# Optimization experiments

Measured on AMD Instinct MI355X. Metric: run time of the kernel, lower is better.

Reference implementation:

```python
import jax, jax.numpy as jnp
import numpy as np

BETA = 0.35

def setup_inputs() -> dict:
    key = jax.random.key(0)
    k1, k2, k3 = jax.random.split(key, 3)
    B, D, C, O = 16384, 512, 4096, 128
    x = jax.random.normal(k1, (B, D), dtype=jnp.float32)
    centers = jax.random.normal(k2, (C, D), dtype=jnp.float32)
    W = jax.random.normal(k3, (C, O), dtype=jnp.float32) * (1.0 / np.sqrt(C))
    b = jnp.zeros((O,), dtype=jnp.float32)
    return {"x": x, "centers": centers, "W": W, "b": b}

def reference(x, centers, W, b):
    # Squared Euclidean distances via the GEMM identity ||a-b||^2 = ||a||^2 + ||b||^2 - 2 a.b
    # (same math as expand_dims/subtract/square/reduce_sum, avoids [B,C,D] intermediate)
    x_sq = jnp.sum(x * x, axis=1, keepdims=True)          # [B,1]
    c_sq = jnp.sum(centers * centers, axis=1)             # [C]
    cross = x @ centers.T                                  # [B,C]
    sq_dist = x_sq + c_sq[None, :] - 2.0 * cross           # [B,C]
    rbf = jnp.exp(-BETA * sq_dist)                         # [B,C]
    return rbf @ W + b                                      # [B,O]
```

## Files before the change

kernel.cpp:

```cpp
#include <hip/hip_runtime.h>
#include <hip/hip_bf16.h>

typedef short bf16x8 __attribute__((ext_vector_type(8)));
typedef float f32x4 __attribute__((ext_vector_type(4)));
typedef float f32x16 __attribute__((ext_vector_type(16)));
typedef long l64x2 __attribute__((ext_vector_type(2)));
typedef unsigned short u16;
typedef unsigned char u8;

#define NB2 (-0.35f * 1.44269504088896340736f)
#define P2C (0.70f * 1.44269504088896340736f)
#define MF8(a,b,c)  __builtin_amdgcn_mfma_f32_32x32x16_fp8_fp8(a, b, c, 0, 0, 0)
#define MFB(a,b,c)  __builtin_amdgcn_mfma_f32_32x32x16_bf16(a, b, c, 0, 0, 0)

__device__ __forceinline__ u16 f2bf(float f) {
  union { float f; unsigned int u; } v; v.f = f;
  unsigned int x = v.u;
  return (u16)((x + 0x7FFFu + ((x >> 16) & 1u)) >> 16);
}

__device__ __forceinline__ unsigned cvtpk(float lo, float hi) {
  unsigned r;
  asm("v_cvt_pk_bf16_f32 %0, %1, %2" : "=v"(r) : "v"(lo), "v"(hi));
  return r;
}

__device__ __forceinline__ void pswap(unsigned &a, unsigned &b) {
  asm volatile("v_permlane32_swap_b32 %0, %1" : "+v"(a), "+v"(b));
}

__device__ __forceinline__ u8 f2e4m3(float f) {
  unsigned int u = __float_as_uint(f);
  u8 s = (u8)((u >> 24) & 0x80u);
  float a = fabsf(f);
  if (a >= 448.f) return s | 0x7E;
  if (a < 0.015625f) return s | (u8)(int)rintf(a * 512.f);
  unsigned int m = u & 0x7fffffffu;
  unsigned int r = m + 0x7FFFFu + ((m >> 20) & 1u);
  return s | (u8)((((r >> 23) - 120u) << 3) | ((r >> 20) & 7u));
}

__device__ __forceinline__ unsigned int pk4(float a, float b, float c, float d) {
#if __has_builtin(__builtin_amdgcn_cvt_pk_fp8_f32)
  int v = __builtin_amdgcn_cvt_pk_fp8_f32(a, b, 0, false);
  v = __builtin_amdgcn_cvt_pk_fp8_f32(c, d, v, true);
  return (unsigned int)v;
#else
  return (unsigned int)f2e4m3(a) | ((unsigned int)f2e4m3(b) << 8)
       | ((unsigned int)f2e4m3(c) << 16) | ((unsigned int)f2e4m3(d) << 24);
#endif
}

#define GLOAD_LDS(g, l) __builtin_amdgcn_global_load_lds( \
    (const __attribute__((address_space(1))) unsigned int*)(g), \
    (__attribute__((address_space(3))) unsigned int*)(l), 16, 0, 0)

__global__ __launch_bounds__(512)
void prep_x8(const float* __restrict__ src, u8* __restrict__ dst,
             float* __restrict__ sq) {
  const int row = blockIdx.x * 8 + (threadIdx.x >> 6);
  const int i6 = threadIdx.x & 63;
  const float4* p = (const float4*)(src + (size_t)row * 512) + i6 * 2;
  float4 a = p[0], b = p[1];
  float ss = a.x*a.x + a.y*a.y + a.z*a.z + a.w*a.w
           + b.x*b.x + b.y*b.y + b.z*b.z + b.w*b.w;
  uint2 o;
  o.x = pk4(a.x, a.y, a.z, a.w);
  o.y = pk4(b.x, b.y, b.z, b.w);
  const int pp = i6 >> 2, sub = (i6 >> 1) & 1, h = i6 & 1;
  const int l = (h << 5) | (row & 31);
  *(uint2*)(dst + (size_t)(row >> 5) * 16384 + pp * 1024 + l * 16 + sub * 8) = o;
  ss += __shfl_xor(ss, 1);  ss += __shfl_xor(ss, 2);
  ss += __shfl_xor(ss, 4);  ss += __shfl_xor(ss, 8);
  ss += __shfl_xor(ss, 16); ss += __shfl_xor(ss, 32);
  if (i6 == 0) sq[row] = ss;
}

__global__ __launch_bounds__(256)
void prep_cen(const float* __restrict__ cen, u8* __restrict__ cfr,
              float* __restrict__ csq) {
  const int t = threadIdx.x;
  const int c = blockIdx.x * 4 + (t >> 6);
  const int i6 = t & 63;
  const float* p = cen + (size_t)c * 512 + i6 * 8;
  float4 a = *(const float4*)p, b = *(const float4*)(p + 4);
  float ss = a.x*a.x + a.y*a.y + a.z*a.z + a.w*a.w
           + b.x*b.x + b.y*b.y + b.z*b.z + b.w*b.w;
  uint2 o;
  o.x = pk4(a.x, a.y, a.z, a.w);
  o.y = pk4(b.x, b.y, b.z, b.w);
  const int pp = i6 >> 2, sub = (i6 >> 1) & 1, h = i6 & 1;
  const int lc = c & 31;
  const int v = (((lc & 7) * 2 + h) ^ ((lc >> 2) & 1));
  *(uint2*)(cfr + (size_t)(c >> 5) * 16384 + pp * 1024 + (lc >> 3) * 256
            + v * 16 + sub * 8) = o;
  ss += __shfl_xor(ss, 1);  ss += __shfl_xor(ss, 2);
  ss += __shfl_xor(ss, 4);  ss += __shfl_xor(ss, 8);
  ss += __shfl_xor(ss, 16); ss += __shfl_xor(ss, 32);
  if (i6 == 0) csq[c] = ss;
}

__global__ __launch_bounds__(256)
void prep_w(const float* __restrict__ W, u8* __restrict__ wt) {
  __shared__ u16 t_[128 * 66];
  const int c0 = blockIdx.x * 64;
  const int t = threadIdx.x;
#pragma unroll
  for (int it = 0; it < 32; ++it) {
    int idx = it * 256 + t;
    int cl = idx >> 7;
    int o  = idx & 127;
    t_[o * 66 + cl] = f2bf(W[(size_t)(c0 + cl) * 128 + o]);
  }
  __syncthreads();
#pragma unroll
  for (int it = 0; it < 4; ++it) {
    int idx = it * 256 + t;
    int o  = idx >> 3;
    int uu = idx & 7;
    int ch = uu >> 2;
    int kt = (uu >> 1) & 1;
    int h  = uu & 1;
    u16* d = (u16*)(wt + ((size_t)(c0 >> 5) + ch) * 8192 + (o >> 5) * 2048
                    + kt * 1024 + (h * 32 + (o & 31)) * 16);
    const u16* s_ = &t_[o * 66 + ch * 32 + kt * 16 + h * 8];
#pragma unroll
    for (int j = 0; j < 8; ++j) d[j] = s_[j];
  }
}

__global__ __launch_bounds__(256)
void init_out(const float* __restrict__ bias, float* __restrict__ out) {
  const int i4 = blockIdx.x * 256 + threadIdx.x;
  float4 b = ((const float4*)bias)[i4 & 31];
  ((float4*)out)[i4] = b;
}

__global__ __launch_bounds__(256, 2)
void rbf_main(const u8* __restrict__ xfs, const u8* __restrict__ cfr,
              const u8* __restrict__ wtgb, const float* __restrict__ csq_g,
              const float* __restrict__ xsq_g, float* __restrict__ out)
{
  __shared__ __align__(16) u8 cs[3][16384];
  __shared__ __align__(16) float csq_l[1024];
  __shared__ __align__(16) float xsq_l[128];

  const int tid = threadIdx.x;
  const int lane = tid & 63;
  const int wv = tid >> 6;
  const int l31 = lane & 31;
  const int h = lane >> 5;
  const int bid = blockIdx.x;
  const int chq = bid & 3;
  const size_t r0 = (size_t)(bid >> 2) * 128;

#define S_CS(cc) do { \
    const u8* sG_ = cfr + ((size_t)(chq * 32 + (cc)) << 14) + tid * 16; \
    u8* sL_ = &cs[(cc) % 3][0] + tid * 16; \
    GLOAD_LDS(sG_,         sL_); \
    GLOAD_LDS(sG_ + 4096,  sL_ + 4096); \
    GLOAD_LDS(sG_ + 8192,  sL_ + 8192); \
    GLOAD_LDS(sG_ + 12288, sL_ + 12288); \
  } while (0)

  if (tid < 32) GLOAD_LDS(xsq_g + r0 + tid * 4, xsq_l + tid * 4);
  GLOAD_LDS(csq_g + chq * 1024 + tid * 4, csq_l + tid * 4);
  S_CS(0);
  S_CS(1);

  l64x2 xf[16];
  {
    const u8* xb = xfs + ((size_t)((bid >> 2) * 4 + wv)) * 16384 + lane * 16;
#pragma unroll
    for (int p = 0; p < 16; ++p)
      xf[p] = *(const l64x2*)(xb + p * 1024);
  }

  asm volatile("s_waitcnt vmcnt(0)" ::: "memory");
  __builtin_amdgcn_s_barrier();
  __builtin_amdgcn_sched_barrier(0);

  const float xn = NB2 * xsq_l[wv * 32 + l31];

  const int cbase = ((l31 >> 3) & 3) * 256
                  + ((((l31 & 7) * 2 + h) ^ ((l31 >> 2) & 1)) << 4);

  const f32x16 z16 = {0,0,0,0,0,0,0,0,0,0,0,0,0,0,0,0};
  f32x16 oa0 = z16, oa1 = z16, oa2 = z16, oa3 = z16;

#pragma unroll 1
  for (int cc = 0; cc < 32; ++cc) {
    const u8* wgb = wtgb + ((size_t)(chq * 32 + cc) << 13) + lane * 16;
    bf16x8 w00 = *(const bf16x8*)(wgb);
    bf16x8 w01 = *(const bf16x8*)(wgb + 1024);
    bf16x8 w10 = *(const bf16x8*)(wgb + 2048);
    bf16x8 w11 = *(const bf16x8*)(wgb + 3072);
    bf16x8 w20 = *(const bf16x8*)(wgb + 4096);
    bf16x8 w21 = *(const bf16x8*)(wgb + 5120);
    bf16x8 w30 = *(const bf16x8*)(wgb + 6144);
    bf16x8 w31 = *(const bf16x8*)(wgb + 7168);
    __builtin_amdgcn_sched_barrier(0);
    if (cc < 30) S_CS(cc + 2);
    __builtin_amdgcn_sched_barrier(0);

    const u8* csb = &cs[cc % 3][0];

    f32x16 s0 = z16, s1 = z16;
#pragma unroll
    for (int p = 0; p < 16; ++p) {
      l64x2 A = *(const l64x2*)(csb + p * 1024 + cbase);
      __builtin_amdgcn_s_setprio(1);
      if (p & 1) {
        s1 = MF8(A[0], xf[p][0], s1);
        s1 = MF8(A[1], xf[p][1], s1);
      } else {
        s0 = MF8(A[0], xf[p][0], s0);
        s0 = MF8(A[1], xf[p][1], s0);
      }
      __builtin_amdgcn_s_setprio(0);
    }

    f32x4 cq0 = *(const f32x4*)(csq_l + cc * 32 + 0  + 4 * h);
    f32x4 cq1 = *(const f32x4*)(csq_l + cc * 32 + 8  + 4 * h);
    f32x4 cq2 = *(const f32x4*)(csq_l + cc * 32 + 16 + 4 * h);
    f32x4 cq3 = *(const f32x4*)(csq_l + cc * 32 + 24 + 4 * h);
    float e[16];
#pragma unroll
    for (int r = 0; r < 16; ++r) {
      const float cq = (r < 4 ? cq0[r] : r < 8 ? cq1[r - 4] : r < 12 ? cq2[r - 8] : cq3[r - 12]);
      e[r] = __builtin_amdgcn_exp2f(fmaf(s0[r] + s1[r], P2C, fmaf(cq, NB2, xn)));
    }
    unsigned P0 = cvtpk(e[0],  e[1]),  P1 = cvtpk(e[2],  e[3]);
    unsigned P2 = cvtpk(e[4],  e[5]),  P3 = cvtpk(e[6],  e[7]);
    unsigned P4 = cvtpk(e[8],  e[9]),  P5 = cvtpk(e[10], e[11]);
    unsigned P6 = cvtpk(e[12], e[13]), P7 = cvtpk(e[14], e[15]);
    pswap(P0, P2); pswap(P1, P3);
    pswap(P4, P6); pswap(P5, P7);
    union { unsigned u[4]; bf16x8 v; } FA, GA;
    FA.u[0] = P0; FA.u[1] = P1; FA.u[2] = P2; FA.u[3] = P3;
    GA.u[0] = P4; GA.u[1] = P5; GA.u[2] = P6; GA.u[3] = P7;

    if (cc < 30) { asm volatile("s_waitcnt vmcnt(4)" ::: "memory"); }
    else         { asm volatile("s_waitcnt vmcnt(0)" ::: "memory"); }
    __builtin_amdgcn_sched_barrier(0);
    __builtin_amdgcn_s_setprio(1);
    oa0 = MFB(FA.v, w00, oa0);
    oa0 = MFB(GA.v, w01, oa0);
    oa1 = MFB(FA.v, w10, oa1);
    oa1 = MFB(GA.v, w11, oa1);
    oa2 = MFB(FA.v, w20, oa2);
    oa2 = MFB(GA.v, w21, oa2);
    oa3 = MFB(FA.v, w30, oa3);
    oa3 = MFB(GA.v, w31, oa3);
    __builtin_amdgcn_s_setprio(0);

    __builtin_amdgcn_s_barrier();
    __builtin_amdgcn_sched_barrier(0);
  }

#pragma unroll
  for (int r = 0; r < 16; ++r) {
    const int m = wv * 32 + (r & 3) + 8 * (r >> 2) + 4 * h;
    float* op = &out[(r0 + m) * 128 + l31];
    atomicAdd(op,      oa0[r]);
    atomicAdd(op + 32, oa1[r]);
    atomicAdd(op + 64, oa2[r]);
    atomicAdd(op + 96, oa3[r]);
  }
#undef S_CS
}

extern "C" void kernel_launch(void* const* d_in, const int* in_sizes, int n_in,
                              void* d_out, int out_size, void* d_ws, size_t ws_size,
                              hipStream_t stream) {
  (void)in_sizes; (void)n_in; (void)out_size; (void)ws_size;
  const float* x   = (const float*)d_in[0];
  const float* cen = (const float*)d_in[1];
  const float* W   = (const float*)d_in[2];
  const float* b   = (const float*)d_in[3];
  u8* xfs = (u8*)d_ws;
  u8* cfr = xfs + (size_t)16384 * 512;
  u8* wtgb = cfr + (size_t)4096 * 512;
  float* csq = (float*)(wtgb + (size_t)128 * 4096 * 2);
  float* xsq = csq + 4096;
  prep_x8<<<2048, 512, 0, stream>>>(x, xfs, xsq);
  prep_cen<<<1024, 256, 0, stream>>>(cen, cfr, csq);
  prep_w<<<64, 256, 0, stream>>>(W, wtgb);
  init_out<<<2048, 256, 0, stream>>>(b, (float*)d_out);
  rbf_main<<<512, 256, 0, stream>>>(xfs, cfr, wtgb, csq, xsq, (float*)d_out);
}
```

Measured before the change: 109.5 us.

## Software-pipeline distance GEMM of next chunk with exp and output GEMM

```diff
diff --git a/kernel.cpp b/kernel.cpp
--- a/kernel.cpp
+++ b/kernel.cpp
@@ -141,7 +141,7 @@
               const u8* __restrict__ wtgb, const float* __restrict__ csq_g,
               const float* __restrict__ xsq_g, float* __restrict__ out)
 {
-  __shared__ __align__(16) u8 cs[3][16384];
+  __shared__ __align__(16) u8 cs[4][16384];
   __shared__ __align__(16) float csq_l[1024];
   __shared__ __align__(16) float xsq_l[128];
 
@@ -156,7 +156,7 @@
 
 #define S_CS(cc) do { \
     const u8* sG_ = cfr + ((size_t)(chq * 32 + (cc)) << 14) + tid * 16; \
-    u8* sL_ = &cs[(cc) % 3][0] + tid * 16; \
+    u8* sL_ = &cs[(cc) & 3][0] + tid * 16; \
     GLOAD_LDS(sG_,         sL_); \
     GLOAD_LDS(sG_ + 4096,  sL_ + 4096); \
     GLOAD_LDS(sG_ + 8192,  sL_ + 8192); \
@@ -181,82 +181,101 @@
   __builtin_amdgcn_sched_barrier(0);
 
   const float xn = NB2 * xsq_l[wv * 32 + l31];
-
   const int cbase = ((l31 >> 3) & 3) * 256
                   + ((((l31 & 7) * 2 + h) ^ ((l31 >> 2) & 1)) << 4);
 
   const f32x16 z16 = {0,0,0,0,0,0,0,0,0,0,0,0,0,0,0,0};
   f32x16 oa0 = z16, oa1 = z16, oa2 = z16, oa3 = z16;
+  f32x16 sA0 = z16, sA1 = z16, sB0 = z16, sB1 = z16;
+
+#define G1Q(Na, Nb, Q, CSB, INIT) do { \
+    l64x2 A0 = *(const l64x2*)((CSB) + (4*(Q)+0)*1024 + cbase); \
+    l64x2 A1 = *(const l64x2*)((CSB) + (4*(Q)+1)*1024 + cbase); \
+    l64x2 A2 = *(const l64x2*)((CSB) + (4*(Q)+2)*1024 + cbase); \
+    l64x2 A3 = *(const l64x2*)((CSB) + (4*(Q)+3)*1024 + cbase); \
+    __builtin_amdgcn_s_setprio(1); \
+    if (INIT) { Na = MF8(A0[0], xf[4*(Q)+0][0], z16); \
+                Nb = MF8(A1[0], xf[4*(Q)+1][0], z16); } \
+    else      { Na = MF8(A0[0], xf[4*(Q)+0][0], Na); \
+                Nb = MF8(A1[0], xf[4*(Q)+1][0], Nb); } \
+    Na = MF8(A0[1], xf[4*(Q)+0][1], Na); \
+    Nb = MF8(A1[1], xf[4*(Q)+1][1], Nb); \
+    Na = MF8(A2[0], xf[4*(Q)+2][0], Na); \
+    Nb = MF8(A3[0], xf[4*(Q)+3][0], Nb); \
+    Na = MF8(A2[1], xf[4*(Q)+2][1], Na); \
+    Nb = MF8(A3[1], xf[4*(Q)+3][1], Nb); \
+    __builtin_amdgcn_s_setprio(0); \
+  } while (0)
+
+#define EXPQ(Ca, Cb, Q, CC, Pa, Pb) do { \
+    f32x4 cqv = *(const f32x4*)(csq_l + (CC) * 32 + (Q) * 8 + 4 * h); \
+    float e0_ = __builtin_amdgcn_exp2f(fmaf((Ca)[4*(Q)+0] + (Cb)[4*(Q)+0], P2C, fmaf(cqv[0], NB2, xn))); \
+    float e1_ = __builtin_amdgcn_exp2f(fmaf((Ca)[4*(Q)+1] + (Cb)[4*(Q)+1], P2C, fmaf(cqv[1], NB2, xn))); \
+    float e2_ = __builtin_amdgcn_exp2f(fmaf((Ca)[4*(Q)+2] + (Cb)[4*(Q)+2], P2C, fmaf(cqv[2], NB2, xn))); \
+    float e3_ = __builtin_amdgcn_exp2f(fmaf((Ca)[4*(Q)+3] + (Cb)[4*(Q)+3], P2C, fmaf(cqv[3], NB2, xn))); \
+    Pa = cvtpk(e0_, e1_); \
+    Pb = cvtpk(e2_, e3_); \
+  } while (0)
+
+#define BODY(CC, Ca, Cb, Na, Nb, VM) do { \
+    asm volatile("s_waitcnt vmcnt(0)" ::: "memory"); \
+    __builtin_amdgcn_s_barrier(); \
+    __builtin_amdgcn_sched_barrier(0); \
+    const u8* wgb = wtgb + ((size_t)(chq * 32 + (CC)) << 13) + lane * 16; \
+    bf16x8 w00 = *(const bf16x8*)(wgb); \
+    bf16x8 w01 = *(const bf16x8*)(wgb + 1024); \
+    bf16x8 w10 = *(const bf16x8*)(wgb + 2048); \
+    bf16x8 w11 = *(const bf16x8*)(wgb + 3072); \
+    bf16x8 w20 = *(const bf16x8*)(wgb + 4096); \
+    bf16x8 w21 = *(const bf16x8*)(wgb + 5120); \
+    bf16x8 w30 = *(const bf16x8*)(wgb + 6144); \
+    bf16x8 w31 = *(const bf16x8*)(wgb + 7168); \
+    if ((CC) + 2 < 32) S_CS((CC) + 2); \
+    __builtin_amdgcn_sched_barrier(0); \
+    const u8* csb = &cs[((CC) + 1) & 3][0]; \
+    unsigned P0, P1, P2, P3, P4, P5, P6, P7; \
+    if ((CC) < 31) G1Q(Na, Nb, 0, csb, 1); \
+    EXPQ(Ca, Cb, 0, CC, P0, P1); \
+    if ((CC) < 31) G1Q(Na, Nb, 1, csb, 0); \
+    EXPQ(Ca, Cb, 1, CC, P2, P3); \
+    if ((CC) < 31) G1Q(Na, Nb, 2, csb, 0); \
+    EXPQ(Ca, Cb, 2, CC, P4, P5); \
+    if ((CC) < 31) G1Q(Na, Nb, 3, csb, 0); \
+    EXPQ(Ca, Cb, 3, CC, P6, P7); \
+    pswap(P0, P2); pswap(P1, P3); \
+    pswap(P4, P6); pswap(P5, P7); \
+    union { unsigned u[4]; bf16x8 v; } FA, GA; \
+    FA.u[0] = P0; FA.u[1] = P1; FA.u[2] = P2; FA.u[3] = P3; \
+    GA.u[0] = P4; GA.u[1] = P5; GA.u[2] = P6; GA.u[3] = P7; \
+    asm volatile("s_waitcnt vmcnt(" #VM ")" ::: "memory"); \
+    __builtin_amdgcn_sched_barrier(0); \
+    __builtin_amdgcn_s_setprio(1); \
+    oa0 = MFB(FA.v, w00, oa0); \
+    oa1 = MFB(FA.v, w10, oa1); \
+    oa2 = MFB(FA.v, w20, oa2); \
+    oa3 = MFB(FA.v, w30, oa3); \
+    oa0 = MFB(GA.v, w01, oa0); \
+    oa1 = MFB(GA.v, w11, oa1); \
+    oa2 = MFB(GA.v, w21, oa2); \
+    oa3 = MFB(GA.v, w31, oa3); \
+    __builtin_amdgcn_s_setprio(0); \
+  } while (0)
+
+  {
+    const u8* csb0 = &cs[0][0];
+    G1Q(sA0, sA1, 0, csb0, 1);
+    G1Q(sA0, sA1, 1, csb0, 0);
+    G1Q(sA0, sA1, 2, csb0, 0);
+    G1Q(sA0, sA1, 3, csb0, 0);
+  }
 
 #pragma unroll 1
-  for (int cc = 0; cc < 32; ++cc) {
-    const u8* wgb = wtgb + ((size_t)(chq * 32 + cc) << 13) + lane * 16;
-    bf16x8 w00 = *(const bf16x8*)(wgb);
-    bf16x8 w01 = *(const bf16x8*)(wgb + 1024);
-    bf16x8 w10 = *(const bf16x8*)(wgb + 2048);
-    bf16x8 w11 = *(const bf16x8*)(wgb + 3072);
-    bf16x8 w20 = *(const bf16x8*)(wgb + 4096);
-    bf16x8 w21 = *(const bf16x8*)(wgb + 5120);
-    bf16x8 w30 = *(const bf16x8*)(wgb + 6144);
-    bf16x8 w31 = *(const bf16x8*)(wgb + 7168);
-    __builtin_amdgcn_sched_barrier(0);
-    if (cc < 30) S_CS(cc + 2);
-    __builtin_amdgcn_sched_barrier(0);
-
-    const u8* csb = &cs[cc % 3][0];
-
-    f32x16 s0 = z16, s1 = z16;
-#pragma unroll
-    for (int p = 0; p < 16; ++p) {
-      l64x2 A = *(const l64x2*)(csb + p * 1024 + cbase);
-      __builtin_amdgcn_s_setprio(1);
-      if (p & 1) {
-        s1 = MF8(A[0], xf[p][0], s1);
-        s1 = MF8(A[1], xf[p][1], s1);
-      } else {
-        s0 = MF8(A[0], xf[p][0], s0);
-        s0 = MF8(A[1], xf[p][1], s0);
-      }
-      __builtin_amdgcn_s_setprio(0);
-    }
-
-    f32x4 cq0 = *(const f32x4*)(csq_l + cc * 32 + 0  + 4 * h);
-    f32x4 cq1 = *(const f32x4*)(csq_l + cc * 32 + 8  + 4 * h);
-    f32x4 cq2 = *(const f32x4*)(csq_l + cc * 32 + 16 + 4 * h);
-    f32x4 cq3 = *(const f32x4*)(csq_l + cc * 32 + 24 + 4 * h);
-    float e[16];
-#pragma unroll
-    for (int r = 0; r < 16; ++r) {
-      const float cq = (r < 4 ? cq0[r] : r < 8 ? cq1[r - 4] : r < 12 ? cq2[r - 8] : cq3[r - 12]);
-      e[r] = __builtin_amdgcn_exp2f(fmaf(s0[r] + s1[r], P2C, fmaf(cq, NB2, xn)));
-    }
-    unsigned P0 = cvtpk(e[0],  e[1]),  P1 = cvtpk(e[2],  e[3]);
-    unsigned P2 = cvtpk(e[4],  e[5]),  P3 = cvtpk(e[6],  e[7]);
-    unsigned P4 = cvtpk(e[8],  e[9]),  P5 = cvtpk(e[10], e[11]);
-    unsigned P6 = cvtpk(e[12], e[13]), P7 = cvtpk(e[14], e[15]);
-    pswap(P0, P2); pswap(P1, P3);
-    pswap(P4, P6); pswap(P5, P7);
-    union { unsigned u[4]; bf16x8 v; } FA, GA;
-    FA.u[0] = P0; FA.u[1] = P1; FA.u[2] = P2; FA.u[3] = P3;
-    GA.u[0] = P4; GA.u[1] = P5; GA.u[2] = P6; GA.u[3] = P7;
-
-    if (cc < 30) { asm volatile("s_waitcnt vmcnt(4)" ::: "memory"); }
-    else         { asm volatile("s_waitcnt vmcnt(0)" ::: "memory"); }
-    __builtin_amdgcn_sched_barrier(0);
-    __builtin_amdgcn_s_setprio(1);
-    oa0 = MFB(FA.v, w00, oa0);
-    oa0 = MFB(GA.v, w01, oa0);
-    oa1 = MFB(FA.v, w10, oa1);
-    oa1 = MFB(GA.v, w11, oa1);
-    oa2 = MFB(FA.v, w20, oa2);
-    oa2 = MFB(GA.v, w21, oa2);
-    oa3 = MFB(FA.v, w30, oa3);
-    oa3 = MFB(GA.v, w31, oa3);
-    __builtin_amdgcn_s_setprio(0);
-
-    __builtin_amdgcn_s_barrier();
-    __builtin_amdgcn_sched_barrier(0);
-  }
+  for (int cc = 0; cc < 30; cc += 2) {
+    BODY(cc,     sA0, sA1, sB0, sB1, 4);
+    BODY(cc + 1, sB0, sB1, sA0, sA1, 4);
+  }
+  BODY(30, sA0, sA1, sB0, sB1, 0);
+  BODY(31, sB0, sB1, sA0, sA1, 0);
 
 #pragma unroll
   for (int r = 0; r < 16; ++r) {
@@ -268,6 +287,9 @@
     atomicAdd(op + 96, oa3[r]);
   }
 #undef S_CS
+#undef G1Q
+#undef EXPQ
+#undef BODY
 }
 
 extern "C" void kernel_launch(void* const* d_in, const int* in_sizes, int n_in,
```

After: 106.2 us. -3.0%, faster.

## Load center fragments directly from global into registers, drop LDS staging

Applied to the files above, without the earlier changes.

```diff
diff --git a/kernel.cpp b/kernel.cpp
--- a/kernel.cpp
+++ b/kernel.cpp
@@ -56,8 +56,8 @@
     (__attribute__((address_space(3))) unsigned int*)(l), 16, 0, 0)
 
 __global__ __launch_bounds__(512)
-void prep_x8(const float* __restrict__ src, u8* __restrict__ dst,
-             float* __restrict__ sq) {
+void prep_f8s(const float* __restrict__ src, u8* __restrict__ dst,
+              float* __restrict__ sq) {
   const int row = blockIdx.x * 8 + (threadIdx.x >> 6);
   const int i6 = threadIdx.x & 63;
   const float4* p = (const float4*)(src + (size_t)row * 512) + i6 * 2;
@@ -77,30 +77,6 @@
 }
 
 __global__ __launch_bounds__(256)
-void prep_cen(const float* __restrict__ cen, u8* __restrict__ cfr,
-              float* __restrict__ csq) {
-  const int t = threadIdx.x;
-  const int c = blockIdx.x * 4 + (t >> 6);
-  const int i6 = t & 63;
-  const float* p = cen + (size_t)c * 512 + i6 * 8;
-  float4 a = *(const float4*)p, b = *(const float4*)(p + 4);
-  float ss = a.x*a.x + a.y*a.y + a.z*a.z + a.w*a.w
-           + b.x*b.x + b.y*b.y + b.z*b.z + b.w*b.w;
-  uint2 o;
-  o.x = pk4(a.x, a.y, a.z, a.w);
-  o.y = pk4(b.x, b.y, b.z, b.w);
-  const int pp = i6 >> 2, sub = (i6 >> 1) & 1, h = i6 & 1;
-  const int lc = c & 31;
-  const int v = (((lc & 7) * 2 + h) ^ ((lc >> 2) & 1));
-  *(uint2*)(cfr + (size_t)(c >> 5) * 16384 + pp * 1024 + (lc >> 3) * 256
-            + v * 16 + sub * 8) = o;
-  ss += __shfl_xor(ss, 1);  ss += __shfl_xor(ss, 2);
-  ss += __shfl_xor(ss, 4);  ss += __shfl_xor(ss, 8);
-  ss += __shfl_xor(ss, 16); ss += __shfl_xor(ss, 32);
-  if (i6 == 0) csq[c] = ss;
-}
-
-__global__ __launch_bounds__(256)
 void prep_w(const float* __restrict__ W, u8* __restrict__ wt) {
   __shared__ u16 t_[128 * 66];
   const int c0 = blockIdx.x * 64;
@@ -136,14 +112,13 @@
   ((float4*)out)[i4] = b;
 }
 
-__global__ __launch_bounds__(256, 2)
+__global__ __launch_bounds__(512, 2)
 void rbf_main(const u8* __restrict__ xfs, const u8* __restrict__ cfr,
-              const u8* __restrict__ wtgb, const float* __restrict__ csq_g,
+              const u8* __restrict__ wfr, const float* __restrict__ csq_g,
               const float* __restrict__ xsq_g, float* __restrict__ out)
 {
-  __shared__ __align__(16) u8 cs[3][16384];
   __shared__ __align__(16) float csq_l[1024];
-  __shared__ __align__(16) float xsq_l[128];
+  __shared__ __align__(16) float xsq_l[256];
 
   const int tid = threadIdx.x;
   const int lane = tid & 63;
@@ -152,25 +127,14 @@
   const int h = lane >> 5;
   const int bid = blockIdx.x;
   const int chq = bid & 3;
-  const size_t r0 = (size_t)(bid >> 2) * 128;
-
-#define S_CS(cc) do { \
-    const u8* sG_ = cfr + ((size_t)(chq * 32 + (cc)) << 14) + tid * 16; \
-    u8* sL_ = &cs[(cc) % 3][0] + tid * 16; \
-    GLOAD_LDS(sG_,         sL_); \
-    GLOAD_LDS(sG_ + 4096,  sL_ + 4096); \
-    GLOAD_LDS(sG_ + 8192,  sL_ + 8192); \
-    GLOAD_LDS(sG_ + 12288, sL_ + 12288); \
-  } while (0)
-
-  if (tid < 32) GLOAD_LDS(xsq_g + r0 + tid * 4, xsq_l + tid * 4);
-  GLOAD_LDS(csq_g + chq * 1024 + tid * 4, csq_l + tid * 4);
-  S_CS(0);
-  S_CS(1);
+  const size_t r0 = (size_t)(bid >> 2) * 256;
+
+  if (tid < 256) GLOAD_LDS(csq_g + chq * 1024 + tid * 4, csq_l + tid * 4);
+  if (tid < 64)  GLOAD_LDS(xsq_g + r0 + tid * 4, xsq_l + tid * 4);
 
   l64x2 xf[16];
   {
-    const u8* xb = xfs + ((size_t)((bid >> 2) * 4 + wv)) * 16384 + lane * 16;
+    const u8* xb = xfs + ((size_t)((bid >> 2) * 8 + wv)) * 16384 + lane * 16;
 #pragma unroll
     for (int p = 0; p < 16; ++p)
       xf[p] = *(const l64x2*)(xb + p * 1024);
@@ -182,15 +146,44 @@
 
   const float xn = NB2 * xsq_l[wv * 32 + l31];
 
-  const int cbase = ((l31 >> 3) & 3) * 256
-                  + ((((l31 & 7) * 2 + h) ^ ((l31 >> 2) & 1)) << 4);
-
   const f32x16 z16 = {0,0,0,0,0,0,0,0,0,0,0,0,0,0,0,0};
   f32x16 oa0 = z16, oa1 = z16, oa2 = z16, oa3 = z16;
 
+#define G1Q(V0, V1, V2, V3, PB) do { \
+    __builtin_amdgcn_s_setprio(1); \
+    s0 = MF8(V0[0], xf[(PB) + 0][0], s0); \
+    s1 = MF8(V0[1], xf[(PB) + 0][1], s1); \
+    s0 = MF8(V1[0], xf[(PB) + 1][0], s0); \
+    s1 = MF8(V1[1], xf[(PB) + 1][1], s1); \
+    s0 = MF8(V2[0], xf[(PB) + 2][0], s0); \
+    s1 = MF8(V2[1], xf[(PB) + 2][1], s1); \
+    s0 = MF8(V3[0], xf[(PB) + 3][0], s0); \
+    s1 = MF8(V3[1], xf[(PB) + 3][1], s1); \
+    __builtin_amdgcn_s_setprio(0); \
+  } while (0)
+
 #pragma unroll 1
   for (int cc = 0; cc < 32; ++cc) {
-    const u8* wgb = wtgb + ((size_t)(chq * 32 + cc) << 13) + lane * 16;
+    const u8* cgb = cfr + ((size_t)(chq * 32 + cc) << 14) + lane * 16;
+    const u8* wgb = wfr + ((size_t)(chq * 32 + cc) << 13) + lane * 16;
+
+    l64x2 A0 = *(const l64x2*)(cgb);
+    l64x2 A1 = *(const l64x2*)(cgb + 1024);
+    l64x2 A2 = *(const l64x2*)(cgb + 2048);
+    l64x2 A3 = *(const l64x2*)(cgb + 3072);
+    l64x2 B0 = *(const l64x2*)(cgb + 4096);
+    l64x2 B1 = *(const l64x2*)(cgb + 5120);
+    l64x2 B2 = *(const l64x2*)(cgb + 6144);
+    l64x2 B3 = *(const l64x2*)(cgb + 7168);
+
+    f32x16 s0 = z16, s1 = z16;
+    G1Q(A0, A1, A2, A3, 0);
+
+    A0 = *(const l64x2*)(cgb + 8192);
+    A1 = *(const l64x2*)(cgb + 9216);
+    A2 = *(const l64x2*)(cgb + 10240);
+    A3 = *(const l64x2*)(cgb + 11264);
+
     bf16x8 w00 = *(const bf16x8*)(wgb);
     bf16x8 w01 = *(const bf16x8*)(wgb + 1024);
     bf16x8 w10 = *(const bf16x8*)(wgb + 2048);
@@ -199,26 +192,16 @@
     bf16x8 w21 = *(const bf16x8*)(wgb + 5120);
     bf16x8 w30 = *(const bf16x8*)(wgb + 6144);
     bf16x8 w31 = *(const bf16x8*)(wgb + 7168);
-    __builtin_amdgcn_sched_barrier(0);
-    if (cc < 30) S_CS(cc + 2);
-    __builtin_amdgcn_sched_barrier(0);
-
-    const u8* csb = &cs[cc % 3][0];
-
-    f32x16 s0 = z16, s1 = z16;
-#pragma unroll
-    for (int p = 0; p < 16; ++p) {
-      l64x2 A = *(const l64x2*)(csb + p * 1024 + cbase);
-      __builtin_amdgcn_s_setprio(1);
-      if (p & 1) {
-        s1 = MF8(A[0], xf[p][0], s1);
-        s1 = MF8(A[1], xf[p][1], s1);
-      } else {
-        s0 = MF8(A[0], xf[p][0], s0);
-        s0 = MF8(A[1], xf[p][1], s0);
-      }
-      __builtin_amdgcn_s_setprio(0);
-    }
+
+    G1Q(B0, B1, B2, B3, 4);
+
+    B0 = *(const l64x2*)(cgb + 12288);
+    B1 = *(const l64x2*)(cgb + 13312);
+    B2 = *(const l64x2*)(cgb + 14336);
+    B3 = *(const l64x2*)(cgb + 15360);
+
+    G1Q(A0, A1, A2, A3, 8);
+    G1Q(B0, B1, B2, B3, 12);
 
     f32x4 cq0 = *(const f32x4*)(csq_l + cc * 32 + 0  + 4 * h);
     f32x4 cq1 = *(const f32x4*)(csq_l + cc * 32 + 8  + 4 * h);
@@ -240,9 +223,6 @@
     FA.u[0] = P0; FA.u[1] = P1; FA.u[2] = P2; FA.u[3] = P3;
     GA.u[0] = P4; GA.u[1] = P5; GA.u[2] = P6; GA.u[3] = P7;
 
-    if (cc < 30) { asm volatile("s_waitcnt vmcnt(4)" ::: "memory"); }
-    else         { asm volatile("s_waitcnt vmcnt(0)" ::: "memory"); }
-    __builtin_amdgcn_sched_barrier(0);
     __builtin_amdgcn_s_setprio(1);
     oa0 = MFB(FA.v, w00, oa0);
     oa0 = MFB(GA.v, w01, oa0);
@@ -253,9 +233,6 @@
     oa3 = MFB(FA.v, w30, oa3);
     oa3 = MFB(GA.v, w31, oa3);
     __builtin_amdgcn_s_setprio(0);
-
-    __builtin_amdgcn_s_barrier();
-    __builtin_amdgcn_sched_barrier(0);
   }
 
 #pragma unroll
@@ -267,7 +244,7 @@
     atomicAdd(op + 64, oa2[r]);
     atomicAdd(op + 96, oa3[r]);
   }
-#undef S_CS
+#undef G1Q
 }
 
 extern "C" void kernel_launch(void* const* d_in, const int* in_sizes, int n_in,
@@ -280,12 +257,12 @@
   const float* b   = (const float*)d_in[3];
   u8* xfs = (u8*)d_ws;
   u8* cfr = xfs + (size_t)16384 * 512;
-  u8* wtgb = cfr + (size_t)4096 * 512;
-  float* csq = (float*)(wtgb + (size_t)128 * 4096 * 2);
+  u8* wfr = cfr + (size_t)4096 * 512;
+  float* csq = (float*)(wfr + (size_t)128 * 8192);
   float* xsq = csq + 4096;
-  prep_x8<<<2048, 512, 0, stream>>>(x, xfs, xsq);
-  prep_cen<<<1024, 256, 0, stream>>>(cen, cfr, csq);
-  prep_w<<<64, 256, 0, stream>>>(W, wtgb);
+  prep_f8s<<<2048, 512, 0, stream>>>(x, xfs, xsq);
+  prep_f8s<<<512, 512, 0, stream>>>(cen, cfr, csq);
+  prep_w<<<64, 256, 0, stream>>>(W, wfr);
   init_out<<<2048, 256, 0, stream>>>(b, (float*)d_out);
-  rbf_main<<<512, 256, 0, stream>>>(xfs, cfr, wtgb, csq, xsq, (float*)d_out);
-}
+  rbf_main<<<256, 512, 0, stream>>>(xfs, cfr, wfr, csq, xsq, (float*)d_out);
+}
```

Result: slower. 114.4 us (+4.4%).
